# Kernel optimization log

Hardware: AMD Instinct MI355X
Metric: run time of the kernel (lower is better)

Reference implementation:

```python
import jax, jax.numpy as jnp
import numpy as np

D_MODEL = 2048
NUM_Q_HEADS = 32
NUM_KV_HEADS = 8
HEAD_DIM = D_MODEL // NUM_Q_HEADS  # 64
DIM_KV = NUM_KV_HEADS * HEAD_DIM   # 512
ROPE_THETA = 500000.0
B, T = 1, 2048


def setup_inputs() -> dict:
    key = jax.random.key(0)
    ks = jax.random.split(key, 7)
    f = lambda k, shape, scale: (jax.random.normal(k, shape, jnp.float32) * scale)
    return {
        "q_embs": f(ks[0], (B, T, D_MODEL), 1.0),
        "k_embs": f(ks[1], (B, T, D_MODEL), 1.0),
        "v_embs": f(ks[2], (B, T, D_MODEL), 1.0),
        "w_q": f(ks[3], (D_MODEL, D_MODEL), 0.02),
        "w_k": f(ks[4], (D_MODEL, DIM_KV), 0.02),
        "w_v": f(ks[5], (D_MODEL, DIM_KV), 0.02),
        "w_o": f(ks[6], (D_MODEL, D_MODEL), 0.02),
    }


def _rope(x):
    # x: (B, H, T, D). Llama-style interleaved rotary embedding.
    Tn, D = x.shape[-2], x.shape[-1]
    inv_freq = 1.0 / (ROPE_THETA ** (jnp.arange(0, D, 2, dtype=jnp.float32) / D))  # (D/2,)
    ang = jnp.arange(Tn, dtype=jnp.float32)[:, None] * inv_freq[None, :]  # (T, D/2)
    cos, sin = jnp.cos(ang), jnp.sin(ang)
    x1, x2 = x[..., ::2], x[..., 1::2]
    # interleave rotated pairs back into last dim
    out = jnp.stack([x1 * cos - x2 * sin, x1 * sin + x2 * cos], axis=-1)
    return out.reshape(x.shape)


def reference(q_embs, k_embs, v_embs, w_q, w_k, w_v, w_o):
    Bn, Tn, _ = q_embs.shape
    # projections, then split heads: (B, T, H*D) -> (B, H, T, D)
    q = (q_embs @ w_q).reshape(Bn, Tn, NUM_Q_HEADS, HEAD_DIM).transpose(0, 2, 1, 3)
    k = (k_embs @ w_k).reshape(Bn, Tn, NUM_KV_HEADS, HEAD_DIM).transpose(0, 2, 1, 3)
    v = (v_embs @ w_v).reshape(Bn, Tn, NUM_KV_HEADS, HEAD_DIM).transpose(0, 2, 1, 3)
    q = _rope(q)
    k = _rope(k)
    # GQA: repeat each kv head n_rep consecutive times (matches torch expand+rearrange)
    n_rep = NUM_Q_HEADS // NUM_KV_HEADS
    k = jnp.repeat(k, n_rep, axis=1)
    v = jnp.repeat(v, n_rep, axis=1)
    scores = jnp.einsum("bhqd,bhkd->bhqk", q, k) * (HEAD_DIM ** -0.5)
    causal = jnp.tril(jnp.ones((Tn, Tn), dtype=bool))
    scores = jnp.where(causal, scores, -jnp.inf)
    wei = jax.nn.softmax(scores, axis=-1)
    out = jnp.einsum("bhqk,bhkd->bhqd", wei, v)
    out = out.transpose(0, 2, 1, 3).reshape(Bn, Tn, NUM_Q_HEADS * HEAD_DIM)
    return out @ w_o
```

## Files before the change

kernel.cpp:

```cpp
#include <hip/hip_runtime.h>
#include <hip/hip_bf16.h>
#include <cstdint>

#define D_MODEL 2048
#define T_SEQ   2048
#define NQH     32
#define NKVH    8
#define HD      64
#define DIM_KV  512

typedef __attribute__((ext_vector_type(8))) __bf16 bf16x8;
typedef __attribute__((ext_vector_type(4))) float  f32x4;
typedef __attribute__((ext_vector_type(4))) unsigned int u32x4;
typedef unsigned short ushort_t;

#define NEG_BIG (-1e30f)
#define AS1 __attribute__((address_space(1)))
#define AS3 __attribute__((address_space(3)))

__device__ __forceinline__ float bf2f(unsigned int u) {
    union { unsigned int i; float f; } v; v.i = u << 16; return v.f;
}
__device__ __forceinline__ ushort_t f2bf(float f) {
    __hip_bfloat16 h = __float2bfloat16(f);
    return *reinterpret_cast<ushort_t*>(&h);
}
__device__ __forceinline__ u32x4 pack8(f32x4 a, f32x4 b) {
    u32x4 r;
    r.x = (unsigned)f2bf(a.x) | ((unsigned)f2bf(a.y) << 16);
    r.y = (unsigned)f2bf(a.z) | ((unsigned)f2bf(a.w) << 16);
    r.z = (unsigned)f2bf(b.x) | ((unsigned)f2bf(b.y) << 16);
    r.w = (unsigned)f2bf(b.z) | ((unsigned)f2bf(b.w) << 16);
    return r;
}
__device__ __forceinline__ void gll16(const ushort_t* g, ushort_t* l) {
    __builtin_amdgcn_global_load_lds((const AS1 void*)g, (AS3 void*)l, 16, 0, 0);
}

__global__ __launch_bounds__(256) void conv3(const float* __restrict__ Xq,
                                             const float* __restrict__ Xk,
                                             const float* __restrict__ Xv,
                                             ushort_t* __restrict__ E) {
    int which = blockIdx.y;
    const float* X = (which == 0) ? Xq : (which == 1) ? Xk : Xv;
    ushort_t* out = E + (size_t)which * (4u * 1024 * 1024);
    int i8 = (blockIdx.x * 256 + threadIdx.x) * 8;
    f32x4 a = *(const f32x4*)(X + i8);
    f32x4 b = *(const f32x4*)(X + i8 + 4);
    *(u32x4*)(out + i8) = pack8(a, b);
}

__global__ __launch_bounds__(256) void transpose_w3(const float* __restrict__ Wq,
                                                    const float* __restrict__ Wk,
                                                    const float* __restrict__ Wv,
                                                    ushort_t* __restrict__ WqT,
                                                    ushort_t* __restrict__ WkT,
                                                    ushort_t* __restrict__ WvT) {
    __shared__ ushort_t tile[64][65];
    int bx = blockIdx.x;
    const float* W; ushort_t* Wt; int N, n0;
    if (bx < 32)      { W = Wq; Wt = WqT; N = 2048; n0 = bx * 64; }
    else if (bx < 40) { W = Wk; Wt = WkT; N = 512;  n0 = (bx - 32) * 64; }
    else              { W = Wv; Wt = WvT; N = 512;  n0 = (bx - 40) * 64; }
    const int K = 2048;
    int k0 = blockIdx.y * 64;
    int tid = threadIdx.x;
#pragma unroll
    for (int ii = 0; ii < 16; ii++) {
        int idx = tid + ii * 256;
        int r = idx >> 6, c = idx & 63;
        tile[r][c] = f2bf(W[(size_t)(k0 + r) * N + n0 + c]);
    }
    __syncthreads();
#pragma unroll
    for (int ii = 0; ii < 16; ii++) {
        int idx = tid + ii * 256;
        int r = idx >> 6, c = idx & 63;
        Wt[(size_t)(n0 + r) * K + k0 + c] = tile[c][r];
    }
}

__global__ __launch_bounds__(256) void transpose_w(const float* __restrict__ W,
                                                   ushort_t* __restrict__ Wt,
                                                   int K, int N) {
    __shared__ ushort_t tile[64][65];
    int n0 = blockIdx.x * 64;
    int k0 = blockIdx.y * 64;
    int tid = threadIdx.x;
#pragma unroll
    for (int ii = 0; ii < 16; ii++) {
        int idx = tid + ii * 256;
        int r = idx >> 6, c = idx & 63;
        tile[r][c] = f2bf(W[(size_t)(k0 + r) * N + n0 + c]);
    }
    __syncthreads();
#pragma unroll
    for (int ii = 0; ii < 16; ii++) {
        int idx = tid + ii * 256;
        int r = idx >> 6, c = idx & 63;
        Wt[(size_t)(n0 + r) * K + k0 + c] = tile[c][r];
    }
}

__global__ __launch_bounds__(256) void transpose_v(const ushort_t* __restrict__ V,
                                                   ushort_t* __restrict__ Vt) {
    __shared__ ushort_t tile[64][65];
    int h  = blockIdx.y;
    int j0 = blockIdx.x * 64;
    int tid = threadIdx.x;
#pragma unroll
    for (int ii = 0; ii < 16; ii++) {
        int idx = tid + ii * 256;
        int r = idx >> 6, c = idx & 63;
        tile[r][c] = V[(size_t)(j0 + r) * DIM_KV + h * HD + c];
    }
    __syncthreads();
#pragma unroll
    for (int ii = 0; ii < 16; ii++) {
        int idx = tid + ii * 256;
        int r = idx >> 6, c = idx & 63;
        Vt[((size_t)h * HD + r) * T_SEQ + j0 + c] = tile[c][r];
    }
}

__global__ __launch_bounds__(256) void gemm_qkv(const ushort_t* __restrict__ Eq,
                                                const ushort_t* __restrict__ Ek,
                                                const ushort_t* __restrict__ Ev,
                                                const ushort_t* __restrict__ wqT,
                                                const ushort_t* __restrict__ wkT,
                                                const ushort_t* __restrict__ wvT,
                                                ushort_t* __restrict__ Qb,
                                                ushort_t* __restrict__ Kb,
                                                ushort_t* __restrict__ Vb) {
    __shared__ ushort_t As[2][64][32];
    __shared__ ushort_t Bs[2][64][32];
    int tid  = threadIdx.x;
    int lane = tid & 63;
    int wave = tid >> 6;

    int b = blockIdx.x;
    int L = (b & 7) * 192 + (b >> 3);
    const ushort_t *A, *Bt; ushort_t* C; int m, n, ldc;
    if (L < 1024) {
        int band = L >> 8, r = L & 255;
        n = r >> 3; m = (band << 3) + (r & 7);
        A = Eq; Bt = wqT; C = Qb; ldc = D_MODEL;
    } else if (L < 1280) {
        int LK = L - 1024; int band = LK >> 6, r = LK & 63;
        n = r >> 3; m = (band << 3) + (r & 7);
        A = Ek; Bt = wkT; C = Kb; ldc = DIM_KV;
    } else {
        int LV = L - 1280; int band = LV >> 6, r = LV & 63;
        n = r >> 3; m = (band << 3) + (r & 7);
        A = Ev; Bt = wvT; C = Vb; ldc = DIM_KV;
    }
    const int K = 2048;
    int m0 = m * 64;
    int n0 = n * 64;
    int wm = (wave >> 1) * 32;
    int wn = (wave & 1) * 32;
    int lrow = tid >> 2;
    int lcol = (tid & 3) * 8;

    f32x4 acc[2][2];
#pragma unroll
    for (int i = 0; i < 2; i++)
#pragma unroll
        for (int j = 0; j < 2; j++) acc[i][j] = (f32x4){0.f, 0.f, 0.f, 0.f};

    const int mrow = lane & 15;
    const int kq   = (lane >> 4) * 8;
    const ushort_t* Arow = A  + (size_t)(m0 + lrow) * K + lcol;
    const ushort_t* Brow = Bt + (size_t)(n0 + lrow) * K + lcol;

    gll16(Arow, &As[0][lrow][lcol]);
    gll16(Brow, &Bs[0][lrow][lcol]);
    __syncthreads();

    int cur = 0;
#pragma unroll 1
    for (int t = 0; t < 64; t++) {
        if (t + 1 < 64) {
            int k1 = (t + 1) << 5;
            gll16(Arow + k1, &As[cur ^ 1][lrow][lcol]);
            gll16(Brow + k1, &Bs[cur ^ 1][lrow][lcol]);
        }
        bf16x8 afr[2], bfr[2];
#pragma unroll
        for (int i = 0; i < 2; i++) afr[i] = *(const bf16x8*)&As[cur][wm + i * 16 + mrow][kq];
#pragma unroll
        for (int j = 0; j < 2; j++) bfr[j] = *(const bf16x8*)&Bs[cur][wn + j * 16 + mrow][kq];
#pragma unroll
        for (int i = 0; i < 2; i++)
#pragma unroll
            for (int j = 0; j < 2; j++)
                acc[i][j] = __builtin_amdgcn_mfma_f32_16x16x32_bf16(afr[i], bfr[j], acc[i][j], 0, 0, 0);
        __syncthreads();
        cur ^= 1;
    }

    int crow = (lane >> 4) * 4;
    int ccol = lane & 15;
#pragma unroll
    for (int i = 0; i < 2; i++)
#pragma unroll
        for (int j = 0; j < 2; j++) {
            int col = n0 + wn + j * 16 + ccol;
#pragma unroll
            for (int r = 0; r < 4; r++) {
                int row = m0 + wm + i * 16 + crow + r;
                C[(size_t)row * ldc + col] = f2bf(acc[i][j][r]);
            }
        }
}

template <int OF32>
__global__ __launch_bounds__(256) void gemm128x64(const ushort_t* __restrict__ A,
                                                  const ushort_t* __restrict__ Bt,
                                                  void* __restrict__ C,
                                                  int M, int N, int K) {
    __shared__ ushort_t As[2][128][32];
    __shared__ ushort_t Bs[2][64][32];
    int tid  = threadIdx.x;
    int lane = tid & 63;
    int wave = tid >> 6;
    int m0 = blockIdx.y * 128;
    int n0 = blockIdx.x * 64;
    int wm = (wave >> 1) * 64;
    int wn = (wave & 1) * 32;
    int lrow = tid >> 2;
    int lcol = (tid & 3) * 8;

    f32x4 acc[4][2];
#pragma unroll
    for (int i = 0; i < 4; i++)
#pragma unroll
        for (int j = 0; j < 2; j++) acc[i][j] = (f32x4){0.f, 0.f, 0.f, 0.f};

    const int mrow = lane & 15;
    const int kq   = (lane >> 4) * 8;

    gll16(A  + (size_t)(m0 + lrow) * K + lcol,      &As[0][lrow][lcol]);
    gll16(A  + (size_t)(m0 + 64 + lrow) * K + lcol, &As[0][64 + lrow][lcol]);
    gll16(Bt + (size_t)(n0 + lrow) * K + lcol,      &Bs[0][lrow][lcol]);
    __syncthreads();

    int nk  = K >> 5;
    int cur = 0;
    for (int t = 0; t < nk; t++) {
        if (t + 1 < nk) {
            int k1 = (t + 1) << 5;
            gll16(A  + (size_t)(m0 + lrow) * K + k1 + lcol,      &As[cur ^ 1][lrow][lcol]);
            gll16(A  + (size_t)(m0 + 64 + lrow) * K + k1 + lcol, &As[cur ^ 1][64 + lrow][lcol]);
            gll16(Bt + (size_t)(n0 + lrow) * K + k1 + lcol,      &Bs[cur ^ 1][lrow][lcol]);
        }
        bf16x8 afr[4], bfr[2];
#pragma unroll
        for (int i = 0; i < 4; i++) afr[i] = *(const bf16x8*)&As[cur][wm + i * 16 + mrow][kq];
#pragma unroll
        for (int j = 0; j < 2; j++) bfr[j] = *(const bf16x8*)&Bs[cur][wn + j * 16 + mrow][kq];
#pragma unroll
        for (int i = 0; i < 4; i++)
#pragma unroll
            for (int j = 0; j < 2; j++)
                acc[i][j] = __builtin_amdgcn_mfma_f32_16x16x32_bf16(afr[i], bfr[j], acc[i][j], 0, 0, 0);
        __syncthreads();
        cur ^= 1;
    }

    int crow = (lane >> 4) * 4;
    int ccol = lane & 15;
#pragma unroll
    for (int i = 0; i < 4; i++)
#pragma unroll
        for (int j = 0; j < 2; j++) {
            int col = n0 + wn + j * 16 + ccol;
#pragma unroll
            for (int r = 0; r < 4; r++) {
                int row = m0 + wm + i * 16 + crow + r;
                if (OF32) ((float*)C)[(size_t)row * N + col] = acc[i][j][r];
                else      ((ushort_t*)C)[(size_t)row * N + col] = f2bf(acc[i][j][r]);
            }
        }
}

__global__ void rope_fused(ushort_t* __restrict__ Qb, ushort_t* __restrict__ Kb) {
    const int NQ = T_SEQ * (D_MODEL / 2);
    const int NK = T_SEQ * (DIM_KV / 2);
    int idx = blockIdx.x * blockDim.x + threadIdx.x;
    ushort_t* X; int cols;
    if (idx < NQ) { X = Qb; cols = D_MODEL; }
    else {
        idx -= NQ;
        if (idx >= NK) return;
        X = Kb; cols = DIM_KV;
    }
    int ppr = cols >> 1;
    int t = idx / ppr;
    int j = idx - t * ppr;
    int i = j & 31;
    int col = ((j >> 5) << 6) + (i << 1);
    float inv = expf(-(float)i * (13.122363377404328f / 32.0f));
    float ang = (float)t * inv;
    float c = cosf(ang), s = sinf(ang);
    size_t base = (size_t)t * cols + col;
    float x1 = bf2f((unsigned int)X[base]);
    float x2 = bf2f((unsigned int)X[base + 1]);
    X[base]     = f2bf(x1 * c - x2 * s);
    X[base + 1] = f2bf(x1 * s + x2 * c);
}

__global__ __launch_bounds__(256) void attn_mfma(const ushort_t* __restrict__ Q,
                                                 const ushort_t* __restrict__ Kb,
                                                 const ushort_t* __restrict__ Vt,
                                                 ushort_t* __restrict__ Ob) {
    __shared__ ushort_t Qs[64][72];
    __shared__ ushort_t Ks[64][72];
    __shared__ ushort_t Vs[64][72];
    __shared__ ushort_t Ps[64][72];

    int tid  = threadIdx.x;
    int lane = tid & 63;
    int wave = tid >> 6;
    int h    = blockIdx.x;
    int hk   = h >> 2;
    int y    = blockIdx.y;
    int qt   = (y < 8) ? y : (y < 16) ? 23 - y : (y < 24) ? y : 55 - y;
    int q0   = qt * 64;
    int l15  = lane & 15;
    int quad = lane >> 4;
    int kq   = quad * 8;

    int r = tid >> 3;
    int c = (tid & 7) * 8;

    *(u32x4*)&Qs[r][c]      = *(const u32x4*)(Q + (size_t)(q0 + r) * D_MODEL + h * HD + c);
    *(u32x4*)&Qs[r + 32][c] = *(const u32x4*)(Q + (size_t)(q0 + r + 32) * D_MODEL + h * HD + c);
    __syncthreads();
    bf16x8 aq0 = *(const bf16x8*)&Qs[wave * 16 + l15][kq];
    bf16x8 aq1 = *(const bf16x8*)&Qs[wave * 16 + l15][kq + 32];

    f32x4 oacc[4];
    float l_i[4];
#pragma unroll
    for (int i = 0; i < 4; i++) {
        oacc[i] = (f32x4){0.f, 0.f, 0.f, 0.f};
        l_i[i] = 0.f;
    }

    u32x4 kr0, kr1, vr0, vr1;
    {
        kr0 = *(const u32x4*)(Kb + (size_t)(0 + r) * DIM_KV + hk * HD + c);
        kr1 = *(const u32x4*)(Kb + (size_t)(32 + r) * DIM_KV + hk * HD + c);
        vr0 = *(const u32x4*)(Vt + ((size_t)hk * HD + r) * T_SEQ + 0 + c);
        vr1 = *(const u32x4*)(Vt + ((size_t)hk * HD + r + 32) * T_SEQ + 0 + c);
    }

    int ntiles = qt + 1;
    for (int jt = 0; jt < ntiles; jt++) {
        __syncthreads();
        *(u32x4*)&Ks[r][c]      = kr0;
        *(u32x4*)&Ks[r + 32][c] = kr1;
        *(u32x4*)&Vs[r][c]      = vr0;
        *(u32x4*)&Vs[r + 32][c] = vr1;
        __syncthreads();
        if (jt + 1 < ntiles) {
            int j0 = (jt + 1) * 64;
            kr0 = *(const u32x4*)(Kb + (size_t)(j0 + r) * DIM_KV + hk * HD + c);
            kr1 = *(const u32x4*)(Kb + (size_t)(j0 + r + 32) * DIM_KV + hk * HD + c);
            vr0 = *(const u32x4*)(Vt + ((size_t)hk * HD + r) * T_SEQ + j0 + c);
            vr1 = *(const u32x4*)(Vt + ((size_t)hk * HD + r + 32) * T_SEQ + j0 + c);
        }

        f32x4 sacc[4];
#pragma unroll
        for (int ct = 0; ct < 4; ct++) {
            bf16x8 bk0 = *(const bf16x8*)&Ks[ct * 16 + l15][kq];
            bf16x8 bk1 = *(const bf16x8*)&Ks[ct * 16 + l15][kq + 32];
            sacc[ct] = __builtin_amdgcn_mfma_f32_16x16x32_bf16(aq0, bk0, (f32x4){0.f,0.f,0.f,0.f}, 0, 0, 0);
            sacc[ct] = __builtin_amdgcn_mfma_f32_16x16x32_bf16(aq1, bk1, sacc[ct], 0, 0, 0);
        }

        bool diag = (jt == ntiles - 1);
#pragma unroll
        for (int reg = 0; reg < 4; reg++) {
            int y2 = quad * 4 + reg;
            float sum = 0.f;
#pragma unroll
            for (int ct = 0; ct < 4; ct++) {
                float sv = sacc[ct][reg] * 0.125f;
                if (diag && (ct * 16 + l15 > wave * 16 + y2)) sv = NEG_BIG;
                float p = __expf(sv);
                sum += p;
                Ps[wave * 16 + y2][ct * 16 + l15] = f2bf(p);
            }
            l_i[reg] += sum;
        }

        bf16x8 ap0 = *(const bf16x8*)&Ps[wave * 16 + l15][kq];
        bf16x8 ap1 = *(const bf16x8*)&Ps[wave * 16 + l15][kq + 32];
#pragma unroll
        for (int dt = 0; dt < 4; dt++) {
            bf16x8 bv0 = *(const bf16x8*)&Vs[dt * 16 + l15][kq];
            bf16x8 bv1 = *(const bf16x8*)&Vs[dt * 16 + l15][kq + 32];
            oacc[dt] = __builtin_amdgcn_mfma_f32_16x16x32_bf16(ap0, bv0, oacc[dt], 0, 0, 0);
            oacc[dt] = __builtin_amdgcn_mfma_f32_16x16x32_bf16(ap1, bv1, oacc[dt], 0, 0, 0);
        }
    }

#pragma unroll
    for (int reg = 0; reg < 4; reg++) {
        float tot = l_i[reg];
#pragma unroll
        for (int off = 1; off < 16; off <<= 1) tot += __shfl_xor(tot, off, 64);
        float inv = (tot > 0.f) ? 1.0f / tot : 0.f;
        int row = q0 + wave * 16 + quad * 4 + reg;
#pragma unroll
        for (int dt = 0; dt < 4; dt++) {
            Ob[(size_t)row * D_MODEL + h * HD + dt * 16 + l15] = f2bf(oacc[dt][reg] * inv);
        }
    }
}

extern "C" void kernel_launch(void* const* d_in, const int* in_sizes, int n_in,
                              void* d_out, int out_size, void* d_ws, size_t ws_size,
                              hipStream_t stream) {
    const float* q_embs = (const float*)d_in[0];
    const float* k_embs = (const float*)d_in[1];
    const float* v_embs = (const float*)d_in[2];
    const float* w_q = (const float*)d_in[3];
    const float* w_k = (const float*)d_in[4];
    const float* w_v = (const float*)d_in[5];
    const float* w_o = (const float*)d_in[6];
    float* out = (float*)d_out;

    const size_t M1 = (size_t)1024 * 1024;
    ushort_t* base = (ushort_t*)d_ws;
    ushort_t* Eq  = base + 0 * M1;
    ushort_t* Ek  = base + 4 * M1;
    ushort_t* Ev  = base + 8 * M1;
    ushort_t* wkT = base + 12 * M1;
    ushort_t* wvT = base + 13 * M1;
    ushort_t* Kb  = base + 14 * M1;
    ushort_t* Vb  = base + 15 * M1;
    ushort_t* Vt  = base + 0 * M1;
    ushort_t* woT = base + 1 * M1;
    ushort_t* Ab  = base + 5 * M1;
    ushort_t* wqT = (ushort_t*)d_out;
    ushort_t* Qb  = (ushort_t*)d_out + 4 * M1;

    dim3 blk(256);

    transpose_w3<<<dim3(48, 32), blk, 0, stream>>>(w_q, w_k, w_v, wqT, wkT, wvT);

    conv3<<<dim3(2048, 3), blk, 0, stream>>>(q_embs, k_embs, v_embs, Eq);

    gemm_qkv<<<dim3(1536), blk, 0, stream>>>(Eq, Ek, Ev, wqT, wkT, wvT,
                                             Qb, Kb, Vb);

    const int NROPE = T_SEQ * (D_MODEL / 2) + T_SEQ * (DIM_KV / 2);
    rope_fused<<<(NROPE + 255) / 256, blk, 0, stream>>>(Qb, Kb);

    transpose_v<<<dim3(32, 8), blk, 0, stream>>>(Vb, Vt);
    transpose_w<<<dim3(32, 32), blk, 0, stream>>>(w_o, woT, 2048, 2048);

    attn_mfma<<<dim3(32, 32), blk, 0, stream>>>(Qb, Kb, Vt, Ab);

    gemm128x64<1><<<dim3(32, 16), blk, 0, stream>>>(Ab, woT, out, 2048, 2048, 2048);
}
```

Baseline: 275.5 us.

## Fuse RoPE into QKV GEMM epilogue and enlarge tile to 128x64

Removes the separate RoPE kernel and applies the rotary rotation in the QKV projection GEMM epilogue, pairing adjacent columns with a lane shuffle. It also grows the GEMM tile from 64x64 to 128x64, halving the grid and giving each wave more MFMAs per LDS load. This saves one launch and a full read-modify-write pass over Q and K. In exchange the epilogue computes sin/cos per element in the GEMM, and the grid has fewer blocks, which lowers occupancy.

```diff
diff --git a/kernel.cpp b/kernel.cpp
--- a/kernel.cpp
+++ b/kernel.cpp
@@ -132,49 +132,51 @@
                                                 ushort_t* __restrict__ Qb,
                                                 ushort_t* __restrict__ Kb,
                                                 ushort_t* __restrict__ Vb) {
-    __shared__ ushort_t As[2][64][32];
+    __shared__ ushort_t As[2][128][32];
     __shared__ ushort_t Bs[2][64][32];
     int tid  = threadIdx.x;
     int lane = tid & 63;
     int wave = tid >> 6;
 
     int b = blockIdx.x;
-    int L = (b & 7) * 192 + (b >> 3);
-    const ushort_t *A, *Bt; ushort_t* C; int m, n, ldc;
-    if (L < 1024) {
-        int band = L >> 8, r = L & 255;
-        n = r >> 3; m = (band << 3) + (r & 7);
+    int L = (b & 7) * 96 + (b >> 3);
+    const ushort_t *A, *Bt; ushort_t* C; int m, n, ldc, which;
+    if (L < 512) {
+        which = 0; int band = L >> 7, r = L & 127;
+        n = r >> 2; m = band * 4 + (r & 3);
         A = Eq; Bt = wqT; C = Qb; ldc = D_MODEL;
-    } else if (L < 1280) {
-        int LK = L - 1024; int band = LK >> 6, r = LK & 63;
-        n = r >> 3; m = (band << 3) + (r & 7);
+    } else if (L < 640) {
+        which = 1; int LK = L - 512; int band = LK >> 5, r = LK & 31;
+        n = r >> 2; m = band * 4 + (r & 3);
         A = Ek; Bt = wkT; C = Kb; ldc = DIM_KV;
     } else {
-        int LV = L - 1280; int band = LV >> 6, r = LV & 63;
-        n = r >> 3; m = (band << 3) + (r & 7);
+        which = 2; int LV = L - 640; int band = LV >> 5, r = LV & 31;
+        n = r >> 2; m = band * 4 + (r & 3);
         A = Ev; Bt = wvT; C = Vb; ldc = DIM_KV;
     }
     const int K = 2048;
-    int m0 = m * 64;
+    int m0 = m * 128;
     int n0 = n * 64;
-    int wm = (wave >> 1) * 32;
+    int wm = (wave >> 1) * 64;
     int wn = (wave & 1) * 32;
     int lrow = tid >> 2;
     int lcol = (tid & 3) * 8;
 
-    f32x4 acc[2][2];
-#pragma unroll
-    for (int i = 0; i < 2; i++)
+    f32x4 acc[4][2];
+#pragma unroll
+    for (int i = 0; i < 4; i++)
 #pragma unroll
         for (int j = 0; j < 2; j++) acc[i][j] = (f32x4){0.f, 0.f, 0.f, 0.f};
 
     const int mrow = lane & 15;
     const int kq   = (lane >> 4) * 8;
-    const ushort_t* Arow = A  + (size_t)(m0 + lrow) * K + lcol;
-    const ushort_t* Brow = Bt + (size_t)(n0 + lrow) * K + lcol;
-
-    gll16(Arow, &As[0][lrow][lcol]);
-    gll16(Brow, &Bs[0][lrow][lcol]);
+    const ushort_t* Arow0 = A  + (size_t)(m0 + lrow) * K + lcol;
+    const ushort_t* Arow1 = A  + (size_t)(m0 + 64 + lrow) * K + lcol;
+    const ushort_t* Brow  = Bt + (size_t)(n0 + lrow) * K + lcol;
+
+    gll16(Arow0, &As[0][lrow][lcol]);
+    gll16(Arow1, &As[0][64 + lrow][lcol]);
+    gll16(Brow,  &Bs[0][lrow][lcol]);
     __syncthreads();
 
     int cur = 0;
@@ -182,16 +184,17 @@
     for (int t = 0; t < 64; t++) {
         if (t + 1 < 64) {
             int k1 = (t + 1) << 5;
-            gll16(Arow + k1, &As[cur ^ 1][lrow][lcol]);
-            gll16(Brow + k1, &Bs[cur ^ 1][lrow][lcol]);
-        }
-        bf16x8 afr[2], bfr[2];
-#pragma unroll
-        for (int i = 0; i < 2; i++) afr[i] = *(const bf16x8*)&As[cur][wm + i * 16 + mrow][kq];
+            gll16(Arow0 + k1, &As[cur ^ 1][lrow][lcol]);
+            gll16(Arow1 + k1, &As[cur ^ 1][64 + lrow][lcol]);
+            gll16(Brow + k1,  &Bs[cur ^ 1][lrow][lcol]);
+        }
+        bf16x8 afr[4], bfr[2];
+#pragma unroll
+        for (int i = 0; i < 4; i++) afr[i] = *(const bf16x8*)&As[cur][wm + i * 16 + mrow][kq];
 #pragma unroll
         for (int j = 0; j < 2; j++) bfr[j] = *(const bf16x8*)&Bs[cur][wn + j * 16 + mrow][kq];
 #pragma unroll
-        for (int i = 0; i < 2; i++)
+        for (int i = 0; i < 4; i++)
 #pragma unroll
             for (int j = 0; j < 2; j++)
                 acc[i][j] = __builtin_amdgcn_mfma_f32_16x16x32_bf16(afr[i], bfr[j], acc[i][j], 0, 0, 0);
@@ -201,15 +204,26 @@
 
     int crow = (lane >> 4) * 4;
     int ccol = lane & 15;
-#pragma unroll
-    for (int i = 0; i < 2; i++)
+    bool rope = (which != 2);
+#pragma unroll
+    for (int ai = 0; ai < 4; ai++)
 #pragma unroll
         for (int j = 0; j < 2; j++) {
-            int col = n0 + wn + j * 16 + ccol;
+            int hcol = wn + j * 16 + ccol;
+            int col  = n0 + hcol;
+            float invf = expf(-(float)(hcol >> 1) * (13.122363377404328f / 32.0f));
 #pragma unroll
             for (int r = 0; r < 4; r++) {
-                int row = m0 + wm + i * 16 + crow + r;
-                C[(size_t)row * ldc + col] = f2bf(acc[i][j][r]);
+                int row = m0 + wm + ai * 16 + crow + r;
+                float v = acc[ai][j][r];
+                if (rope) {
+                    float partner = __shfl_xor(v, 1, 64);
+                    float ang = (float)row * invf;
+                    float cs = cosf(ang), sn = sinf(ang);
+                    v = (ccol & 1) ? (partner * sn + v * cs)
+                                   : (v * cs - partner * sn);
+                }
+                C[(size_t)row * ldc + col] = f2bf(v);
             }
         }
 }
@@ -284,32 +298,6 @@
         }
 }
 
-__global__ void rope_fused(ushort_t* __restrict__ Qb, ushort_t* __restrict__ Kb) {
-    const int NQ = T_SEQ * (D_MODEL / 2);
-    const int NK = T_SEQ * (DIM_KV / 2);
-    int idx = blockIdx.x * blockDim.x + threadIdx.x;
-    ushort_t* X; int cols;
-    if (idx < NQ) { X = Qb; cols = D_MODEL; }
-    else {
-        idx -= NQ;
-        if (idx >= NK) return;
-        X = Kb; cols = DIM_KV;
-    }
-    int ppr = cols >> 1;
-    int t = idx / ppr;
-    int j = idx - t * ppr;
-    int i = j & 31;
-    int col = ((j >> 5) << 6) + (i << 1);
-    float inv = expf(-(float)i * (13.122363377404328f / 32.0f));
-    float ang = (float)t * inv;
-    float c = cosf(ang), s = sinf(ang);
-    size_t base = (size_t)t * cols + col;
-    float x1 = bf2f((unsigned int)X[base]);
-    float x2 = bf2f((unsigned int)X[base + 1]);
-    X[base]     = f2bf(x1 * c - x2 * s);
-    X[base + 1] = f2bf(x1 * s + x2 * c);
-}
-
 __global__ __launch_bounds__(256) void attn_mfma(const ushort_t* __restrict__ Q,
                                                  const ushort_t* __restrict__ Kb,
                                                  const ushort_t* __restrict__ Vt,
@@ -455,11 +443,8 @@
 
     conv3<<<dim3(2048, 3), blk, 0, stream>>>(q_embs, k_embs, v_embs, Eq);
 
-    gemm_qkv<<<dim3(1536), blk, 0, stream>>>(Eq, Ek, Ev, wqT, wkT, wvT,
-                                             Qb, Kb, Vb);
-
-    const int NROPE = T_SEQ * (D_MODEL / 2) + T_SEQ * (DIM_KV / 2);
-    rope_fused<<<(NROPE + 255) / 256, blk, 0, stream>>>(Qb, Kb);
+    gemm_qkv<<<dim3(768), blk, 0, stream>>>(Eq, Ek, Ev, wqT, wkT, wvT,
+                                            Qb, Kb, Vb);
 
     transpose_v<<<dim3(32, 8), blk, 0, stream>>>(Vb, Vt);
     transpose_w<<<dim3(32, 32), blk, 0, stream>>>(w_o, woT, 2048, 2048);
```

Result: no change. 275.4 us (-0.0%).

## Fuse RoPE into QKV GEMM epilogue and merge prep/transpose kernels

Applied to the files above, without the earlier changes.

Applies the rotary embedding in the QKV GEMM epilogue, using a lane shuffle to fetch each pair partner, which removes the separate RoPE pass over Q and K. The conversion and weight-transpose kernels are merged into one launch, as are the V transpose and the w_o transpose. The output projection GEMM moves to 64x64 tiles with a swizzled block order. This cuts launch count and an extra read-write of Q and K, but adds cos/sin work to the GEMM epilogue, and the smaller output tiles reduce data reuse.

```diff
diff --git a/kernel.cpp b/kernel.cpp
--- a/kernel.cpp
+++ b/kernel.cpp
@@ -37,34 +37,39 @@
     __builtin_amdgcn_global_load_lds((const AS1 void*)g, (AS3 void*)l, 16, 0, 0);
 }
 
-__global__ __launch_bounds__(256) void conv3(const float* __restrict__ Xq,
-                                             const float* __restrict__ Xk,
-                                             const float* __restrict__ Xv,
-                                             ushort_t* __restrict__ E) {
-    int which = blockIdx.y;
-    const float* X = (which == 0) ? Xq : (which == 1) ? Xk : Xv;
-    ushort_t* out = E + (size_t)which * (4u * 1024 * 1024);
-    int i8 = (blockIdx.x * 256 + threadIdx.x) * 8;
-    f32x4 a = *(const f32x4*)(X + i8);
-    f32x4 b = *(const f32x4*)(X + i8 + 4);
-    *(u32x4*)(out + i8) = pack8(a, b);
-}
-
-__global__ __launch_bounds__(256) void transpose_w3(const float* __restrict__ Wq,
-                                                    const float* __restrict__ Wk,
-                                                    const float* __restrict__ Wv,
-                                                    ushort_t* __restrict__ WqT,
-                                                    ushort_t* __restrict__ WkT,
-                                                    ushort_t* __restrict__ WvT) {
+__global__ __launch_bounds__(256) void prep(const float* __restrict__ Xq,
+                                            const float* __restrict__ Xk,
+                                            const float* __restrict__ Xv,
+                                            ushort_t* __restrict__ E,
+                                            const float* __restrict__ Wq,
+                                            const float* __restrict__ Wk,
+                                            const float* __restrict__ Wv,
+                                            ushort_t* __restrict__ WqT,
+                                            ushort_t* __restrict__ WkT,
+                                            ushort_t* __restrict__ WvT) {
     __shared__ ushort_t tile[64][65];
-    int bx = blockIdx.x;
+    int b = blockIdx.x;
+    int tid = threadIdx.x;
+    if (b < 6144) {
+        int which = b >> 11;
+        int bx    = b & 2047;
+        const float* X = (which == 0) ? Xq : (which == 1) ? Xk : Xv;
+        ushort_t* out = E + (size_t)which * (4u * 1024 * 1024);
+        int i8 = (bx * 256 + tid) * 8;
+        f32x4 a = *(const f32x4*)(X + i8);
+        f32x4 c = *(const f32x4*)(X + i8 + 4);
+        *(u32x4*)(out + i8) = pack8(a, c);
+        return;
+    }
+    int t  = b - 6144;
+    int bx = t % 48;
+    int by = t / 48;
     const float* W; ushort_t* Wt; int N, n0;
     if (bx < 32)      { W = Wq; Wt = WqT; N = 2048; n0 = bx * 64; }
     else if (bx < 40) { W = Wk; Wt = WkT; N = 512;  n0 = (bx - 32) * 64; }
     else              { W = Wv; Wt = WvT; N = 512;  n0 = (bx - 40) * 64; }
     const int K = 2048;
-    int k0 = blockIdx.y * 64;
-    int tid = threadIdx.x;
+    int k0 = by * 64;
 #pragma unroll
     for (int ii = 0; ii < 16; ii++) {
         int idx = tid + ii * 256;
@@ -80,46 +85,47 @@
     }
 }
 
-__global__ __launch_bounds__(256) void transpose_w(const float* __restrict__ W,
-                                                   ushort_t* __restrict__ Wt,
-                                                   int K, int N) {
+__global__ __launch_bounds__(256) void posttrans(const ushort_t* __restrict__ Vb,
+                                                 ushort_t* __restrict__ Vt,
+                                                 const float* __restrict__ Wo,
+                                                 ushort_t* __restrict__ WoT) {
     __shared__ ushort_t tile[64][65];
-    int n0 = blockIdx.x * 64;
-    int k0 = blockIdx.y * 64;
+    int b = blockIdx.x;
     int tid = threadIdx.x;
+    if (b < 256) {
+        int h  = b >> 5;
+        int j0 = (b & 31) * 64;
+#pragma unroll
+        for (int ii = 0; ii < 16; ii++) {
+            int idx = tid + ii * 256;
+            int r = idx >> 6, c = idx & 63;
+            tile[r][c] = Vb[(size_t)(j0 + r) * DIM_KV + h * HD + c];
+        }
+        __syncthreads();
+#pragma unroll
+        for (int ii = 0; ii < 16; ii++) {
+            int idx = tid + ii * 256;
+            int r = idx >> 6, c = idx & 63;
+            Vt[((size_t)h * HD + r) * T_SEQ + j0 + c] = tile[c][r];
+        }
+        return;
+    }
+    int t  = b - 256;
+    int n0 = (t & 31) * 64;
+    int k0 = (t >> 5) * 64;
+    const int K = 2048, N = 2048;
 #pragma unroll
     for (int ii = 0; ii < 16; ii++) {
         int idx = tid + ii * 256;
         int r = idx >> 6, c = idx & 63;
-        tile[r][c] = f2bf(W[(size_t)(k0 + r) * N + n0 + c]);
+        tile[r][c] = f2bf(Wo[(size_t)(k0 + r) * N + n0 + c]);
     }
     __syncthreads();
 #pragma unroll
     for (int ii = 0; ii < 16; ii++) {
         int idx = tid + ii * 256;
         int r = idx >> 6, c = idx & 63;
-        Wt[(size_t)(n0 + r) * K + k0 + c] = tile[c][r];
-    }
-}
-
-__global__ __launch_bounds__(256) void transpose_v(const ushort_t* __restrict__ V,
-                                                   ushort_t* __restrict__ Vt) {
-    __shared__ ushort_t tile[64][65];
-    int h  = blockIdx.y;
-    int j0 = blockIdx.x * 64;
-    int tid = threadIdx.x;
-#pragma unroll
-    for (int ii = 0; ii < 16; ii++) {
-        int idx = tid + ii * 256;
-        int r = idx >> 6, c = idx & 63;
-        tile[r][c] = V[(size_t)(j0 + r) * DIM_KV + h * HD + c];
-    }
-    __syncthreads();
-#pragma unroll
-    for (int ii = 0; ii < 16; ii++) {
-        int idx = tid + ii * 256;
-        int r = idx >> 6, c = idx & 63;
-        Vt[((size_t)h * HD + r) * T_SEQ + j0 + c] = tile[c][r];
+        WoT[(size_t)(n0 + r) * K + k0 + c] = tile[c][r];
     }
 }
 
@@ -140,17 +146,17 @@
 
     int b = blockIdx.x;
     int L = (b & 7) * 192 + (b >> 3);
-    const ushort_t *A, *Bt; ushort_t* C; int m, n, ldc;
+    const ushort_t *A, *Bt; ushort_t* C; int m, n, ldc, which;
     if (L < 1024) {
-        int band = L >> 8, r = L & 255;
+        which = 0; int band = L >> 8, r = L & 255;
         n = r >> 3; m = (band << 3) + (r & 7);
         A = Eq; Bt = wqT; C = Qb; ldc = D_MODEL;
     } else if (L < 1280) {
-        int LK = L - 1024; int band = LK >> 6, r = LK & 63;
+        which = 1; int LK = L - 1024; int band = LK >> 6, r = LK & 63;
         n = r >> 3; m = (band << 3) + (r & 7);
         A = Ek; Bt = wkT; C = Kb; ldc = DIM_KV;
     } else {
-        int LV = L - 1280; int band = LV >> 6, r = LV & 63;
+        which = 2; int LV = L - 1280; int band = LV >> 6, r = LV & 63;
         n = r >> 3; m = (band << 3) + (r & 7);
         A = Ev; Bt = wvT; C = Vb; ldc = DIM_KV;
     }
@@ -201,66 +207,81 @@
 
     int crow = (lane >> 4) * 4;
     int ccol = lane & 15;
-#pragma unroll
-    for (int i = 0; i < 2; i++)
+    bool rope = (which != 2);
+#pragma unroll
+    for (int ai = 0; ai < 2; ai++)
 #pragma unroll
         for (int j = 0; j < 2; j++) {
-            int col = n0 + wn + j * 16 + ccol;
+            int hcol = wn + j * 16 + ccol;
+            int col  = n0 + hcol;
+            float invf = expf(-(float)(hcol >> 1) * (13.122363377404328f / 32.0f));
 #pragma unroll
             for (int r = 0; r < 4; r++) {
-                int row = m0 + wm + i * 16 + crow + r;
-                C[(size_t)row * ldc + col] = f2bf(acc[i][j][r]);
+                int row = m0 + wm + ai * 16 + crow + r;
+                float v = acc[ai][j][r];
+                if (rope) {
+                    float partner = __shfl_xor(v, 1, 64);
+                    float ang = (float)row * invf;
+                    float cs = cosf(ang), sn = sinf(ang);
+                    v = (ccol & 1) ? (partner * sn + v * cs)
+                                   : (v * cs - partner * sn);
+                }
+                C[(size_t)row * ldc + col] = f2bf(v);
             }
         }
 }
 
-template <int OF32>
-__global__ __launch_bounds__(256) void gemm128x64(const ushort_t* __restrict__ A,
-                                                  const ushort_t* __restrict__ Bt,
-                                                  void* __restrict__ C,
-                                                  int M, int N, int K) {
-    __shared__ ushort_t As[2][128][32];
+__global__ __launch_bounds__(256) void gemm_o(const ushort_t* __restrict__ A,
+                                              const ushort_t* __restrict__ Bt,
+                                              float* __restrict__ C) {
+    __shared__ ushort_t As[2][64][32];
     __shared__ ushort_t Bs[2][64][32];
     int tid  = threadIdx.x;
     int lane = tid & 63;
     int wave = tid >> 6;
-    int m0 = blockIdx.y * 128;
-    int n0 = blockIdx.x * 64;
-    int wm = (wave >> 1) * 64;
+
+    int b = blockIdx.x;
+    int L = (b & 7) * 128 + (b >> 3);
+    int band = L >> 8, r = L & 255;
+    int n = r >> 3, m = (band << 3) + (r & 7);
+    const int K = 2048, N = 2048;
+    int m0 = m * 64;
+    int n0 = n * 64;
+    int wm = (wave >> 1) * 32;
     int wn = (wave & 1) * 32;
     int lrow = tid >> 2;
     int lcol = (tid & 3) * 8;
 
-    f32x4 acc[4][2];
-#pragma unroll
-    for (int i = 0; i < 4; i++)
+    f32x4 acc[2][2];
+#pragma unroll
+    for (int i = 0; i < 2; i++)
 #pragma unroll
         for (int j = 0; j < 2; j++) acc[i][j] = (f32x4){0.f, 0.f, 0.f, 0.f};
 
     const int mrow = lane & 15;
     const int kq   = (lane >> 4) * 8;
-
-    gll16(A  + (size_t)(m0 + lrow) * K + lcol,      &As[0][lrow][lcol]);
-    gll16(A  + (size_t)(m0 + 64 + lrow) * K + lcol, &As[0][64 + lrow][lcol]);
-    gll16(Bt + (size_t)(n0 + lrow) * K + lcol,      &Bs[0][lrow][lcol]);
+    const ushort_t* Arow = A  + (size_t)(m0 + lrow) * K + lcol;
+    const ushort_t* Brow = Bt + (size_t)(n0 + lrow) * K + lcol;
+
+    gll16(Arow, &As[0][lrow][lcol]);
+    gll16(Brow, &Bs[0][lrow][lcol]);
     __syncthreads();
 
-    int nk  = K >> 5;
     int cur = 0;
-    for (int t = 0; t < nk; t++) {
-        if (t + 1 < nk) {
+#pragma unroll 1
+    for (int t = 0; t < 64; t++) {
+        if (t + 1 < 64) {
             int k1 = (t + 1) << 5;
-            gll16(A  + (size_t)(m0 + lrow) * K + k1 + lcol,      &As[cur ^ 1][lrow][lcol]);
-            gll16(A  + (size_t)(m0 + 64 + lrow) * K + k1 + lcol, &As[cur ^ 1][64 + lrow][lcol]);
-            gll16(Bt + (size_t)(n0 + lrow) * K + k1 + lcol,      &Bs[cur ^ 1][lrow][lcol]);
-        }
-        bf16x8 afr[4], bfr[2];
-#pragma unroll
-        for (int i = 0; i < 4; i++) afr[i] = *(const bf16x8*)&As[cur][wm + i * 16 + mrow][kq];
+            gll16(Arow + k1, &As[cur ^ 1][lrow][lcol]);
+            gll16(Brow + k1, &Bs[cur ^ 1][lrow][lcol]);
+        }
+        bf16x8 afr[2], bfr[2];
+#pragma unroll
+        for (int i = 0; i < 2; i++) afr[i] = *(const bf16x8*)&As[cur][wm + i * 16 + mrow][kq];
 #pragma unroll
         for (int j = 0; j < 2; j++) bfr[j] = *(const bf16x8*)&Bs[cur][wn + j * 16 + mrow][kq];
 #pragma unroll
-        for (int i = 0; i < 4; i++)
+        for (int i = 0; i < 2; i++)
 #pragma unroll
             for (int j = 0; j < 2; j++)
                 acc[i][j] = __builtin_amdgcn_mfma_f32_16x16x32_bf16(afr[i], bfr[j], acc[i][j], 0, 0, 0);
@@ -271,43 +292,16 @@
     int crow = (lane >> 4) * 4;
     int ccol = lane & 15;
 #pragma unroll
-    for (int i = 0; i < 4; i++)
+    for (int i = 0; i < 2; i++)
 #pragma unroll
         for (int j = 0; j < 2; j++) {
             int col = n0 + wn + j * 16 + ccol;
 #pragma unroll
             for (int r = 0; r < 4; r++) {
                 int row = m0 + wm + i * 16 + crow + r;
-                if (OF32) ((float*)C)[(size_t)row * N + col] = acc[i][j][r];
-                else      ((ushort_t*)C)[(size_t)row * N + col] = f2bf(acc[i][j][r]);
+                C[(size_t)row * N + col] = acc[i][j][r];
             }
         }
-}
-
-__global__ void rope_fused(ushort_t* __restrict__ Qb, ushort_t* __restrict__ Kb) {
-    const int NQ = T_SEQ * (D_MODEL / 2);
-    const int NK = T_SEQ * (DIM_KV / 2);
-    int idx = blockIdx.x * blockDim.x + threadIdx.x;
-    ushort_t* X; int cols;
-    if (idx < NQ) { X = Qb; cols = D_MODEL; }
-    else {
-        idx -= NQ;
-        if (idx >= NK) return;
-        X = Kb; cols = DIM_KV;
-    }
-    int ppr = cols >> 1;
-    int t = idx / ppr;
-    int j = idx - t * ppr;
-    int i = j & 31;
-    int col = ((j >> 5) << 6) + (i << 1);
-    float inv = expf(-(float)i * (13.122363377404328f / 32.0f));
-    float ang = (float)t * inv;
-    float c = cosf(ang), s = sinf(ang);
-    size_t base = (size_t)t * cols + col;
-    float x1 = bf2f((unsigned int)X[base]);
-    float x2 = bf2f((unsigned int)X[base + 1]);
-    X[base]     = f2bf(x1 * c - x2 * s);
-    X[base + 1] = f2bf(x1 * s + x2 * c);
 }
 
 __global__ __launch_bounds__(256) void attn_mfma(const ushort_t* __restrict__ Q,
@@ -451,20 +445,15 @@
 
     dim3 blk(256);
 
-    transpose_w3<<<dim3(48, 32), blk, 0, stream>>>(w_q, w_k, w_v, wqT, wkT, wvT);
-
-    conv3<<<dim3(2048, 3), blk, 0, stream>>>(q_embs, k_embs, v_embs, Eq);
+    prep<<<dim3(6144 + 1536), blk, 0, stream>>>(q_embs, k_embs, v_embs, Eq,
+                                                w_q, w_k, w_v, wqT, wkT, wvT);
 
     gemm_qkv<<<dim3(1536), blk, 0, stream>>>(Eq, Ek, Ev, wqT, wkT, wvT,
                                              Qb, Kb, Vb);
 
-    const int NROPE = T_SEQ * (D_MODEL / 2) + T_SEQ * (DIM_KV / 2);
-    rope_fused<<<(NROPE + 255) / 256, blk, 0, stream>>>(Qb, Kb);
-
-    transpose_v<<<dim3(32, 8), blk, 0, stream>>>(Vb, Vt);
-    transpose_w<<<dim3(32, 32), blk, 0, stream>>>(w_o, woT, 2048, 2048);
+    posttrans<<<dim3(256 + 1024), blk, 0, stream>>>(Vb, Vt, w_o, woT);
 
     attn_mfma<<<dim3(32, 32), blk, 0, stream>>>(Qb, Kb, Vt, Ab);
 
-    gemm128x64<1><<<dim3(32, 16), blk, 0, stream>>>(Ab, woT, out, 2048, 2048, 2048);
-}
+    gemm_o<<<dim3(1024), blk, 0, stream>>>(Ab, woT, out);
+}
```

Measured after the change: 263.7 us. 1.04x faster.
